# Kernel optimization log

Measured on AMD Instinct MI355X. Metric: run time of the kernel, lower is better.

The kernel has to match this reference:

```python
import jax, jax.numpy as jnp
import numpy as np
import math

N_HEADS, INPUT_DIM, EMBED_DIM = 8, 128, 128
KEY_DIM = EMBED_DIM // N_HEADS  # val_dim = key_dim = 16
B, N = 4, 512


def setup_inputs() -> dict:
    key = jax.random.key(0)
    ks = jax.random.split(key, 8)
    stdv_k = 1.0 / math.sqrt(KEY_DIM)
    stdv_e = 1.0 / math.sqrt(EMBED_DIM)
    stdv_1 = 1.0
    q = jax.random.normal(ks[0], (B, N, INPUT_DIM), dtype=jnp.float32)
    e = jax.random.normal(ks[1], (B, N, N, INPUT_DIM), dtype=jnp.float32)
    W_query = jax.random.uniform(ks[2], (N_HEADS, INPUT_DIM, KEY_DIM), jnp.float32, -stdv_k, stdv_k)
    W_key = jax.random.uniform(ks[3], (N_HEADS, INPUT_DIM, KEY_DIM), jnp.float32, -stdv_k, stdv_k)
    W_val = jax.random.uniform(ks[4], (N_HEADS, INPUT_DIM, KEY_DIM), jnp.float32, -stdv_k, stdv_k)
    E_val1 = jax.random.uniform(ks[5], (N_HEADS, INPUT_DIM, 1), jnp.float32, -stdv_1, stdv_1)
    W_out = jax.random.uniform(ks[6], (N_HEADS, KEY_DIM, EMBED_DIM), jnp.float32, -stdv_e, stdv_e)
    return {"q": q, "e": e, "W_query": W_query, "W_key": W_key,
            "W_val": W_val, "E_val1": E_val1, "W_out": W_out}


def reference(q, e, W_query, W_key, W_val, E_val1, W_out):
    # h = q (self-attention); shapes: q [B,N,D], e [B,N,N,D]
    norm = 1.0 / math.sqrt(W_query.shape[-1])
    Q = jnp.einsum('bnd,hdk->hbnk', q, W_query)  # [H,B,N,k]
    K = jnp.einsum('bnd,hdk->hbnk', q, W_key)
    V = jnp.einsum('bnd,hdv->hbnv', q, W_val)
    # edge bias: per-head scalar projection of edge features -> [H,B,N,N]
    E = jnp.einsum('bnmd,hd->hbnm', e, E_val1[..., 0])
    compat = norm * jnp.einsum('hbnk,hbmk->hbnm', Q, K) + E
    attn = jax.nn.softmax(compat, axis=-1)
    heads = jnp.einsum('hbnm,hbmv->hbnv', attn, V)
    out = jnp.einsum('hbnv,hve->bne', heads, W_out)  # [B,N,embed]
    return out
```

## Files before the change

kernel.cpp:

```cpp
#include <hip/hip_runtime.h>
#include <math.h>

#define BB 4
#define NN 512
#define DD 128
#define HH 8
#define KK 16

__global__ __launch_bounds__(128) void proj_kernel(
    const float* __restrict__ q,
    const float* __restrict__ Wq,
    const float* __restrict__ Wk,
    const float* __restrict__ Wv,
    float* __restrict__ Qs,
    float* __restrict__ Kp,
    float* __restrict__ Vp)
{
    __shared__ float qrow[DD];
    const int bn = blockIdx.x;
    const int t = threadIdx.x;
    qrow[t] = q[(size_t)bn * DD + t];
    __syncthreads();
    const int h = t >> 4;
    const int k = t & 15;
    const float* wq = Wq + (size_t)h * DD * KK + k;
    const float* wk = Wk + (size_t)h * DD * KK + k;
    const float* wv = Wv + (size_t)h * DD * KK + k;
    float aq = 0.f, ak = 0.f, av = 0.f;
#pragma unroll 16
    for (int d = 0; d < DD; ++d) {
        const float x = qrow[d];
        aq = fmaf(x, wq[(size_t)d * KK], aq);
        ak = fmaf(x, wk[(size_t)d * KK], ak);
        av = fmaf(x, wv[(size_t)d * KK], av);
    }
    Qs[(size_t)bn * DD + t] = aq * 0.25f;
    Kp[(size_t)bn * DD + t] = ak;
    Vp[(size_t)bn * DD + t] = av;
}

__global__ __launch_bounds__(256) void attn_kernel(
    const float* __restrict__ e,
    const float* __restrict__ Ev,
    const float* __restrict__ Qs,
    const float* __restrict__ Kp,
    const float* __restrict__ Vp,
    const float* __restrict__ Wout,
    float* __restrict__ out)
{
    __shared__ float comp[HH][NN + 4];
    __shared__ float headsv[HH * KK];

    const int bn   = blockIdx.x;
    const int b    = bn >> 9;
    const int tid  = threadIdx.x;
    const int wave = tid >> 6;
    const int lane = tid & 63;
    const int sub  = lane >> 4;
    const int dc   = lane & 15;
    const int d0   = dc * 8;
    const int myh  = dc >> 1;

    float ev[HH][8];
#pragma unroll
    for (int h = 0; h < HH; ++h) {
        const float4 a = *(const float4*)(Ev + h * DD + d0);
        const float4 c = *(const float4*)(Ev + h * DD + d0 + 4);
        ev[h][0] = a.x; ev[h][1] = a.y; ev[h][2] = a.z; ev[h][3] = a.w;
        ev[h][4] = c.x; ev[h][5] = c.y; ev[h][6] = c.z; ev[h][7] = c.w;
    }
    float qf[8];
    {
        const float4 a = *(const float4*)(Qs + (size_t)bn * DD + d0);
        const float4 c = *(const float4*)(Qs + (size_t)bn * DD + d0 + 4);
        qf[0] = a.x; qf[1] = a.y; qf[2] = a.z; qf[3] = a.w;
        qf[4] = c.x; qf[5] = c.y; qf[6] = c.z; qf[7] = c.w;
    }

    const float* ebase = e  + (size_t)bn * NN * DD;
    const float* kbase = Kp + (size_t)b  * NN * DD;

    for (int i = 0; i < 32; ++i) {
        const int m = wave * 128 + i * 4 + sub;
        const float* ep  = ebase + (size_t)m * DD + d0;
        const float* kpp = kbase + (size_t)m * DD + d0;
        const float4 e0 = *(const float4*)(ep);
        const float4 e1 = *(const float4*)(ep + 4);
        const float4 k0 = *(const float4*)(kpp);
        const float4 k1 = *(const float4*)(kpp + 4);
        float er[8], kr[8];
        er[0] = e0.x; er[1] = e0.y; er[2] = e0.z; er[3] = e0.w;
        er[4] = e1.x; er[5] = e1.y; er[6] = e1.z; er[7] = e1.w;
        kr[0] = k0.x; kr[1] = k0.y; kr[2] = k0.z; kr[3] = k0.w;
        kr[4] = k1.x; kr[5] = k1.y; kr[6] = k1.z; kr[7] = k1.w;

        float kq = 0.f;
#pragma unroll
        for (int j = 0; j < 8; ++j) kq = fmaf(kr[j], qf[j], kq);

        float acc[HH];
#pragma unroll
        for (int h = 0; h < HH; ++h) {
            float s = (myh == h) ? kq : 0.f;
#pragma unroll
            for (int j = 0; j < 8; ++j) s = fmaf(er[j], ev[h][j], s);
            acc[h] = s;
        }

        const bool hi8 = (dc & 8) != 0;
        float t4[4];
#pragma unroll
        for (int j = 0; j < 4; ++j) {
            const float keep = hi8 ? acc[j + 4] : acc[j];
            const float send = hi8 ? acc[j]     : acc[j + 4];
            t4[j] = keep + __shfl_xor(send, 8);
        }
        const bool hi4 = (dc & 4) != 0;
        float t2[2];
#pragma unroll
        for (int j = 0; j < 2; ++j) {
            const float keep = hi4 ? t2[0]*0.f + t4[j + 2] : t4[j];
            const float send = hi4 ? t4[j]     : t4[j + 2];
            t2[j] = keep + __shfl_xor(send, 4);
        }
        const bool hi2 = (dc & 2) != 0;
        float w;
        {
            const float keep = hi2 ? t2[1] : t2[0];
            const float send = hi2 ? t2[0] : t2[1];
            w = keep + __shfl_xor(send, 2);
        }
        w += __shfl_xor(w, 1);
        if ((dc & 1) == 0) comp[dc >> 1][m] = w;
    }
    __syncthreads();

    const float* vbase = Vp + (size_t)b * NN * DD;
#pragma unroll
    for (int hh = 0; hh < 2; ++hh) {
        const int h = wave * 2 + hh;
        float mx = -3.0e38f;
#pragma unroll
        for (int i = 0; i < 8; ++i) mx = fmaxf(mx, comp[h][lane + i * 64]);
#pragma unroll
        for (int mask = 1; mask <= 32; mask <<= 1)
            mx = fmaxf(mx, __shfl_xor(mx, mask));

        float psum = 0.f;
        float av[KK];
#pragma unroll
        for (int v = 0; v < KK; ++v) av[v] = 0.f;
#pragma unroll
        for (int i = 0; i < 8; ++i) {
            const int m = lane + i * 64;
            const float p = __expf(comp[h][m] - mx);
            psum += p;
            const float* vp = vbase + (size_t)m * DD + h * KK;
            const float4 v0 = *(const float4*)(vp);
            const float4 v1 = *(const float4*)(vp + 4);
            const float4 v2 = *(const float4*)(vp + 8);
            const float4 v3 = *(const float4*)(vp + 12);
            av[0]  = fmaf(p, v0.x, av[0]);  av[1]  = fmaf(p, v0.y, av[1]);
            av[2]  = fmaf(p, v0.z, av[2]);  av[3]  = fmaf(p, v0.w, av[3]);
            av[4]  = fmaf(p, v1.x, av[4]);  av[5]  = fmaf(p, v1.y, av[5]);
            av[6]  = fmaf(p, v1.z, av[6]);  av[7]  = fmaf(p, v1.w, av[7]);
            av[8]  = fmaf(p, v2.x, av[8]);  av[9]  = fmaf(p, v2.y, av[9]);
            av[10] = fmaf(p, v2.z, av[10]); av[11] = fmaf(p, v2.w, av[11]);
            av[12] = fmaf(p, v3.x, av[12]); av[13] = fmaf(p, v3.y, av[13]);
            av[14] = fmaf(p, v3.z, av[14]); av[15] = fmaf(p, v3.w, av[15]);
        }
#pragma unroll
        for (int mask = 1; mask <= 32; mask <<= 1)
            psum += __shfl_xor(psum, mask);

        const bool s5 = (lane & 32) != 0;
        float a8[8];
#pragma unroll
        for (int j = 0; j < 8; ++j) {
            const float keep = s5 ? av[j + 8] : av[j];
            const float send = s5 ? av[j]     : av[j + 8];
            a8[j] = keep + __shfl_xor(send, 32);
        }
        const bool s4 = (lane & 16) != 0;
        float a4[4];
#pragma unroll
        for (int j = 0; j < 4; ++j) {
            const float keep = s4 ? a8[j + 4] : a8[j];
            const float send = s4 ? a8[j]     : a8[j + 4];
            a4[j] = keep + __shfl_xor(send, 16);
        }
        const bool s3 = (lane & 8) != 0;
        float a2[2];
#pragma unroll
        for (int j = 0; j < 2; ++j) {
            const float keep = s3 ? a4[j + 2] : a4[j];
            const float send = s3 ? a4[j]     : a4[j + 2];
            a2[j] = keep + __shfl_xor(send, 8);
        }
        const bool s2 = (lane & 4) != 0;
        float a1;
        {
            const float keep = s2 ? a2[1] : a2[0];
            const float send = s2 ? a2[0] : a2[1];
            a1 = keep + __shfl_xor(send, 4);
        }
        a1 += __shfl_xor(a1, 2);
        a1 += __shfl_xor(a1, 1);
        if ((lane & 3) == 0)
            headsv[h * KK + (lane >> 2)] = a1 / psum;
    }
    __syncthreads();

    if (tid < DD) {
        float o = 0.f;
#pragma unroll 8
        for (int p = 0; p < HH * KK; ++p)
            o = fmaf(headsv[p], Wout[(size_t)p * DD + tid], o);
        out[(size_t)bn * DD + tid] = o;
    }
}

extern "C" void kernel_launch(void* const* d_in, const int* in_sizes, int n_in,
                              void* d_out, int out_size, void* d_ws, size_t ws_size,
                              hipStream_t stream) {
    const float* q    = (const float*)d_in[0];
    const float* e    = (const float*)d_in[1];
    const float* Wq   = (const float*)d_in[2];
    const float* Wk   = (const float*)d_in[3];
    const float* Wv   = (const float*)d_in[4];
    const float* Ev   = (const float*)d_in[5];
    const float* Wout = (const float*)d_in[6];
    float* out = (float*)d_out;

    float* Qs = (float*)d_ws;
    float* Kp = Qs + (size_t)BB * NN * DD;
    float* Vp = Kp + (size_t)BB * NN * DD;

    proj_kernel<<<BB * NN, 128, 0, stream>>>(q, Wq, Wk, Wv, Qs, Kp, Vp);
    attn_kernel<<<BB * NN, 256, 0, stream>>>(e, Ev, Qs, Kp, Vp, Wout, out);
}
```

Baseline: 222.5 us.

## Remap edge-score lanes to float4 per row and software-pipeline loads

The edge/key scoring loop now has each lane handle 4 features (32 lanes per row, 2 rows per wave pass) instead of 8. Loads are double-buffered in registers so the next pair of rows is fetched while the current pair is reduced. The launch bounds also ask for 4 blocks per SM to cap register use. This is meant to hide global-memory latency on the large edge tensor, in exchange for more shuffle steps per row and tighter register pressure.

```diff
diff --git a/kernel.cpp b/kernel.cpp
--- a/kernel.cpp
+++ b/kernel.cpp
@@ -39,7 +39,7 @@
     Vp[(size_t)bn * DD + t] = av;
 }
 
-__global__ __launch_bounds__(256) void attn_kernel(
+__global__ __launch_bounds__(256, 4) void attn_kernel(
     const float* __restrict__ e,
     const float* __restrict__ Ev,
     const float* __restrict__ Qs,
@@ -56,83 +56,92 @@
     const int tid  = threadIdx.x;
     const int wave = tid >> 6;
     const int lane = tid & 63;
-    const int sub  = lane >> 4;
-    const int dc   = lane & 15;
-    const int d0   = dc * 8;
-    const int myh  = dc >> 1;
-
-    float ev[HH][8];
+    const int r    = lane >> 5;
+    const int c    = lane & 31;
+    const int d0   = c * 4;
+    const int myh  = c >> 2;
+    const int hidx = (c >> 2) & 7;
+
+    float ev[HH][4];
 #pragma unroll
     for (int h = 0; h < HH; ++h) {
         const float4 a = *(const float4*)(Ev + h * DD + d0);
-        const float4 c = *(const float4*)(Ev + h * DD + d0 + 4);
         ev[h][0] = a.x; ev[h][1] = a.y; ev[h][2] = a.z; ev[h][3] = a.w;
-        ev[h][4] = c.x; ev[h][5] = c.y; ev[h][6] = c.z; ev[h][7] = c.w;
-    }
-    float qf[8];
-    {
-        const float4 a = *(const float4*)(Qs + (size_t)bn * DD + d0);
-        const float4 c = *(const float4*)(Qs + (size_t)bn * DD + d0 + 4);
-        qf[0] = a.x; qf[1] = a.y; qf[2] = a.z; qf[3] = a.w;
-        qf[4] = c.x; qf[5] = c.y; qf[6] = c.z; qf[7] = c.w;
-    }
-
-    const float* ebase = e  + (size_t)bn * NN * DD;
-    const float* kbase = Kp + (size_t)b  * NN * DD;
-
-    for (int i = 0; i < 32; ++i) {
-        const int m = wave * 128 + i * 4 + sub;
-        const float* ep  = ebase + (size_t)m * DD + d0;
-        const float* kpp = kbase + (size_t)m * DD + d0;
-        const float4 e0 = *(const float4*)(ep);
-        const float4 e1 = *(const float4*)(ep + 4);
-        const float4 k0 = *(const float4*)(kpp);
-        const float4 k1 = *(const float4*)(kpp + 4);
-        float er[8], kr[8];
-        er[0] = e0.x; er[1] = e0.y; er[2] = e0.z; er[3] = e0.w;
-        er[4] = e1.x; er[5] = e1.y; er[6] = e1.z; er[7] = e1.w;
-        kr[0] = k0.x; kr[1] = k0.y; kr[2] = k0.z; kr[3] = k0.w;
-        kr[4] = k1.x; kr[5] = k1.y; kr[6] = k1.z; kr[7] = k1.w;
-
-        float kq = 0.f;
-#pragma unroll
-        for (int j = 0; j < 8; ++j) kq = fmaf(kr[j], qf[j], kq);
-
+    }
+    const float4 qf = *(const float4*)(Qs + (size_t)bn * DD + d0);
+
+    const int mb = wave * 128 + r;
+    const float* epl = e  + (size_t)bn * NN * DD + (size_t)mb * DD + d0;
+    const float* kpl = Kp + (size_t)b  * NN * DD + (size_t)mb * DD + d0;
+
+    const bool f16 = (c & 16) != 0;
+    const bool f8  = (c & 8)  != 0;
+    const bool f4  = (c & 4)  != 0;
+
+    auto do_pass = [&](const float4 ee, const float4 kk, const int m) {
+        float kq;
+        kq = kk.x * qf.x;
+        kq = fmaf(kk.y, qf.y, kq);
+        kq = fmaf(kk.z, qf.z, kq);
+        kq = fmaf(kk.w, qf.w, kq);
         float acc[HH];
 #pragma unroll
         for (int h = 0; h < HH; ++h) {
             float s = (myh == h) ? kq : 0.f;
-#pragma unroll
-            for (int j = 0; j < 8; ++j) s = fmaf(er[j], ev[h][j], s);
+            s = fmaf(ee.x, ev[h][0], s);
+            s = fmaf(ee.y, ev[h][1], s);
+            s = fmaf(ee.z, ev[h][2], s);
+            s = fmaf(ee.w, ev[h][3], s);
             acc[h] = s;
         }
-
-        const bool hi8 = (dc & 8) != 0;
         float t4[4];
 #pragma unroll
         for (int j = 0; j < 4; ++j) {
-            const float keep = hi8 ? acc[j + 4] : acc[j];
-            const float send = hi8 ? acc[j]     : acc[j + 4];
-            t4[j] = keep + __shfl_xor(send, 8);
-        }
-        const bool hi4 = (dc & 4) != 0;
+            const float keep = f16 ? acc[j + 4] : acc[j];
+            const float send = f16 ? acc[j]     : acc[j + 4];
+            t4[j] = keep + __shfl_xor(send, 16);
+        }
         float t2[2];
 #pragma unroll
         for (int j = 0; j < 2; ++j) {
-            const float keep = hi4 ? t2[0]*0.f + t4[j + 2] : t4[j];
-            const float send = hi4 ? t4[j]     : t4[j + 2];
-            t2[j] = keep + __shfl_xor(send, 4);
-        }
-        const bool hi2 = (dc & 2) != 0;
+            const float keep = f8 ? t4[j + 2] : t4[j];
+            const float send = f8 ? t4[j]     : t4[j + 2];
+            t2[j] = keep + __shfl_xor(send, 8);
+        }
         float w;
         {
-            const float keep = hi2 ? t2[1] : t2[0];
-            const float send = hi2 ? t2[0] : t2[1];
-            w = keep + __shfl_xor(send, 2);
-        }
+            const float keep = f4 ? t2[1] : t2[0];
+            const float send = f4 ? t2[0] : t2[1];
+            w = keep + __shfl_xor(send, 4);
+        }
+        w += __shfl_xor(w, 2);
         w += __shfl_xor(w, 1);
-        if ((dc & 1) == 0) comp[dc >> 1][m] = w;
-    }
+        if ((c & 3) == 0) comp[hidx][m] = w;
+    };
+
+#define LDF4(p, base) (*(const float4*)((base) + (size_t)(p) * 256))
+
+    float4 ea0 = LDF4(0, epl), ea1 = LDF4(1, epl);
+    float4 ka0 = LDF4(0, kpl), ka1 = LDF4(1, kpl);
+    float4 eb0, eb1, kb0, kb1;
+
+    for (int g = 0; g < 32; g += 2) {
+        {
+            const int p0 = 2 * g + 2, p1 = 2 * g + 3;
+            eb0 = LDF4(p0, epl); eb1 = LDF4(p1, epl);
+            kb0 = LDF4(p0, kpl); kb1 = LDF4(p1, kpl);
+        }
+        do_pass(ea0, ka0, mb + 4 * g);
+        do_pass(ea1, ka1, mb + 4 * g + 2);
+        if (g + 2 < 32) {
+            const int p0 = 2 * g + 4, p1 = 2 * g + 5;
+            ea0 = LDF4(p0, epl); ea1 = LDF4(p1, epl);
+            ka0 = LDF4(p0, kpl); ka1 = LDF4(p1, kpl);
+        }
+        do_pass(eb0, kb0, mb + 4 * g + 4);
+        do_pass(eb1, kb1, mb + 4 * g + 6);
+    }
+#undef LDF4
     __syncthreads();
 
     const float* vbase = Vp + (size_t)b * NN * DD;
```

After: 229.8 us. 1.03x slower.

## Precompute QK^T and transposed V; software-pipeline edge-feature loads in attention

Applied to the files above, without the earlier changes.

Moves the per-head Q·K dot products into a separate kernel that reuses four query rows per block, so the attention kernel streams only the edge tensor in its main loop. V is transposed so the softmax-weighted sum reads coalesced rows. The edge loads are triple-buffered in registers to overlap memory latency with the per-head reductions. In exchange it adds two kernel launches and writes and reads a QK^T buffer of B*N*H*N floats (about 32 MB) to workspace.

```diff
diff --git a/kernel.cpp b/kernel.cpp
--- a/kernel.cpp
+++ b/kernel.cpp
@@ -39,12 +39,78 @@
     Vp[(size_t)bn * DD + t] = av;
 }
 
+__global__ __launch_bounds__(256) void vt_kernel(
+    const float* __restrict__ Vp, float* __restrict__ Vt)
+{
+    __shared__ float tile[64][129];
+    const int b  = blockIdx.x >> 3;
+    const int m0 = (blockIdx.x & 7) * 64;
+    const int t  = threadIdx.x;
+    const float* src = Vp + ((size_t)b * NN + m0) * DD;
+#pragma unroll
+    for (int j = 0; j < 8; ++j) {
+        const int idx4 = t + j * 256;
+        const float4 v = *(const float4*)(src + (size_t)idx4 * 4);
+        const int r = idx4 >> 5, c = (idx4 & 31) * 4;
+        tile[r][c] = v.x; tile[r][c+1] = v.y; tile[r][c+2] = v.z; tile[r][c+3] = v.w;
+    }
+    __syncthreads();
+    const int m = t & 63;
+#pragma unroll
+    for (int p0 = 0; p0 < 128; p0 += 4) {
+        const int p = p0 + (t >> 6);
+        Vt[((size_t)b * DD + p) * NN + m0 + m] = tile[m][p];
+    }
+}
+
+__global__ __launch_bounds__(256) void qkt_kernel(
+    const float* __restrict__ Qs, const float* __restrict__ Kp,
+    float* __restrict__ QKT)
+{
+    const int b    = blockIdx.x >> 7;
+    const int n4   = blockIdx.x & 127;
+    const int tid  = threadIdx.x;
+    const int wave = tid >> 6;
+    const int lane = tid & 63;
+    const int sub  = lane >> 4;
+    const int dc   = lane & 15;
+    const int d0   = dc * 8;
+
+    float qf[4][8];
+#pragma unroll
+    for (int j = 0; j < 4; ++j) {
+        const float* qp = Qs + ((size_t)b * NN + n4 * 4 + j) * DD + d0;
+        const float4 a = *(const float4*)qp;
+        const float4 c = *(const float4*)(qp + 4);
+        qf[j][0]=a.x; qf[j][1]=a.y; qf[j][2]=a.z; qf[j][3]=a.w;
+        qf[j][4]=c.x; qf[j][5]=c.y; qf[j][6]=c.z; qf[j][7]=c.w;
+    }
+    const float* kbase = Kp + (size_t)b * NN * DD;
+    for (int i = 0; i < 32; ++i) {
+        const int m = wave * 128 + i * 4 + sub;
+        const float* kp = kbase + (size_t)m * DD + d0;
+        const float4 k0 = *(const float4*)kp;
+        const float4 k1 = *(const float4*)(kp + 4);
+        float kr[8];
+        kr[0]=k0.x; kr[1]=k0.y; kr[2]=k0.z; kr[3]=k0.w;
+        kr[4]=k1.x; kr[5]=k1.y; kr[6]=k1.z; kr[7]=k1.w;
+#pragma unroll
+        for (int j = 0; j < 4; ++j) {
+            float s = kr[0] * qf[j][0];
+#pragma unroll
+            for (int u = 1; u < 8; ++u) s = fmaf(kr[u], qf[j][u], s);
+            s += __shfl_xor(s, 1);
+            if ((dc & 1) == 0)
+                QKT[(((size_t)b * NN + n4 * 4 + j) * HH + (dc >> 1)) * NN + m] = s;
+        }
+    }
+}
+
 __global__ __launch_bounds__(256) void attn_kernel(
     const float* __restrict__ e,
     const float* __restrict__ Ev,
-    const float* __restrict__ Qs,
-    const float* __restrict__ Kp,
-    const float* __restrict__ Vp,
+    const float* __restrict__ QKT,
+    const float* __restrict__ Vt,
     const float* __restrict__ Wout,
     float* __restrict__ out)
 {
@@ -59,55 +125,34 @@
     const int sub  = lane >> 4;
     const int dc   = lane & 15;
     const int d0   = dc * 8;
-    const int myh  = dc >> 1;
 
     float ev[HH][8];
 #pragma unroll
     for (int h = 0; h < HH; ++h) {
         const float4 a = *(const float4*)(Ev + h * DD + d0);
         const float4 c = *(const float4*)(Ev + h * DD + d0 + 4);
-        ev[h][0] = a.x; ev[h][1] = a.y; ev[h][2] = a.z; ev[h][3] = a.w;
-        ev[h][4] = c.x; ev[h][5] = c.y; ev[h][6] = c.z; ev[h][7] = c.w;
-    }
-    float qf[8];
-    {
-        const float4 a = *(const float4*)(Qs + (size_t)bn * DD + d0);
-        const float4 c = *(const float4*)(Qs + (size_t)bn * DD + d0 + 4);
-        qf[0] = a.x; qf[1] = a.y; qf[2] = a.z; qf[3] = a.w;
-        qf[4] = c.x; qf[5] = c.y; qf[6] = c.z; qf[7] = c.w;
-    }
-
-    const float* ebase = e  + (size_t)bn * NN * DD;
-    const float* kbase = Kp + (size_t)b  * NN * DD;
-
-    for (int i = 0; i < 32; ++i) {
-        const int m = wave * 128 + i * 4 + sub;
-        const float* ep  = ebase + (size_t)m * DD + d0;
-        const float* kpp = kbase + (size_t)m * DD + d0;
-        const float4 e0 = *(const float4*)(ep);
-        const float4 e1 = *(const float4*)(ep + 4);
-        const float4 k0 = *(const float4*)(kpp);
-        const float4 k1 = *(const float4*)(kpp + 4);
-        float er[8], kr[8];
-        er[0] = e0.x; er[1] = e0.y; er[2] = e0.z; er[3] = e0.w;
-        er[4] = e1.x; er[5] = e1.y; er[6] = e1.z; er[7] = e1.w;
-        kr[0] = k0.x; kr[1] = k0.y; kr[2] = k0.z; kr[3] = k0.w;
-        kr[4] = k1.x; kr[5] = k1.y; kr[6] = k1.z; kr[7] = k1.w;
-
-        float kq = 0.f;
-#pragma unroll
-        for (int j = 0; j < 8; ++j) kq = fmaf(kr[j], qf[j], kq);
-
+        ev[h][0]=a.x; ev[h][1]=a.y; ev[h][2]=a.z; ev[h][3]=a.w;
+        ev[h][4]=c.x; ev[h][5]=c.y; ev[h][6]=c.z; ev[h][7]=c.w;
+    }
+
+    const bool hi8 = (dc & 8) != 0;
+    const bool hi4 = (dc & 4) != 0;
+    const bool hi2 = (dc & 2) != 0;
+    const float* epl = e + (size_t)bn * NN * DD
+                         + (size_t)(wave * 128 + sub) * DD + d0;
+
+    auto do_pass = [&](const float4 e0, const float4 e1, const int p) {
+        float er[8];
+        er[0]=e0.x; er[1]=e0.y; er[2]=e0.z; er[3]=e0.w;
+        er[4]=e1.x; er[5]=e1.y; er[6]=e1.z; er[7]=e1.w;
         float acc[HH];
 #pragma unroll
         for (int h = 0; h < HH; ++h) {
-            float s = (myh == h) ? kq : 0.f;
-#pragma unroll
-            for (int j = 0; j < 8; ++j) s = fmaf(er[j], ev[h][j], s);
+            float s = er[0] * ev[h][0];
+#pragma unroll
+            for (int u = 1; u < 8; ++u) s = fmaf(er[u], ev[h][u], s);
             acc[h] = s;
         }
-
-        const bool hi8 = (dc & 8) != 0;
         float t4[4];
 #pragma unroll
         for (int j = 0; j < 4; ++j) {
@@ -115,15 +160,13 @@
             const float send = hi8 ? acc[j]     : acc[j + 4];
             t4[j] = keep + __shfl_xor(send, 8);
         }
-        const bool hi4 = (dc & 4) != 0;
         float t2[2];
 #pragma unroll
         for (int j = 0; j < 2; ++j) {
-            const float keep = hi4 ? t2[0]*0.f + t4[j + 2] : t4[j];
+            const float keep = hi4 ? t4[j + 2] : t4[j];
             const float send = hi4 ? t4[j]     : t4[j + 2];
             t2[j] = keep + __shfl_xor(send, 4);
         }
-        const bool hi2 = (dc & 2) != 0;
         float w;
         {
             const float keep = hi2 ? t2[1] : t2[0];
@@ -131,43 +174,54 @@
             w = keep + __shfl_xor(send, 2);
         }
         w += __shfl_xor(w, 1);
-        if ((dc & 1) == 0) comp[dc >> 1][m] = w;
-    }
-    __syncthreads();
-
-    const float* vbase = Vp + (size_t)b * NN * DD;
+        if ((dc & 1) == 0) comp[dc >> 1][wave * 128 + p * 4 + sub] = w;
+    };
+
+#define LDE(B0, B1, p) { const float* _p = epl + (size_t)(p) * 512; \
+                         B0 = *(const float4*)_p; B1 = *(const float4*)(_p + 4); }
+
+    float4 A0, A1, B0, B1, C0, C1;
+    LDE(A0, A1, 0); LDE(B0, B1, 1);
+    for (int p = 0; p < 30; p += 3) {
+        LDE(C0, C1, p + 2); do_pass(A0, A1, p);
+        LDE(A0, A1, p + 3); do_pass(B0, B1, p + 1);
+        LDE(B0, B1, p + 4); do_pass(C0, C1, p + 2);
+    }
+    do_pass(A0, A1, 30); do_pass(B0, B1, 31);
+#undef LDE
+    __syncthreads();
+
 #pragma unroll
     for (int hh = 0; hh < 2; ++hh) {
         const int h = wave * 2 + hh;
-        float mx = -3.0e38f;
-#pragma unroll
-        for (int i = 0; i < 8; ++i) mx = fmaxf(mx, comp[h][lane + i * 64]);
+        const float* qk   = QKT + ((size_t)bn * HH + h) * NN;
+        const float* vrow = Vt + ((size_t)b * DD + h * KK) * NN;
+
+        float s[8];
+#pragma unroll
+        for (int i = 0; i < 8; ++i)
+            s[i] = comp[h][lane + i * 64] + qk[lane + i * 64];
+
+        float mx = s[0];
+#pragma unroll
+        for (int i = 1; i < 8; ++i) mx = fmaxf(mx, s[i]);
 #pragma unroll
         for (int mask = 1; mask <= 32; mask <<= 1)
             mx = fmaxf(mx, __shfl_xor(mx, mask));
 
-        float psum = 0.f;
+        float pr[8], psum = 0.f;
+#pragma unroll
+        for (int i = 0; i < 8; ++i) { pr[i] = __expf(s[i] - mx); psum += pr[i]; }
+
         float av[KK];
 #pragma unroll
         for (int v = 0; v < KK; ++v) av[v] = 0.f;
 #pragma unroll
-        for (int i = 0; i < 8; ++i) {
-            const int m = lane + i * 64;
-            const float p = __expf(comp[h][m] - mx);
-            psum += p;
-            const float* vp = vbase + (size_t)m * DD + h * KK;
-            const float4 v0 = *(const float4*)(vp);
-            const float4 v1 = *(const float4*)(vp + 4);
-            const float4 v2 = *(const float4*)(vp + 8);
-            const float4 v3 = *(const float4*)(vp + 12);
-            av[0]  = fmaf(p, v0.x, av[0]);  av[1]  = fmaf(p, v0.y, av[1]);
-            av[2]  = fmaf(p, v0.z, av[2]);  av[3]  = fmaf(p, v0.w, av[3]);
-            av[4]  = fmaf(p, v1.x, av[4]);  av[5]  = fmaf(p, v1.y, av[5]);
-            av[6]  = fmaf(p, v1.z, av[6]);  av[7]  = fmaf(p, v1.w, av[7]);
-            av[8]  = fmaf(p, v2.x, av[8]);  av[9]  = fmaf(p, v2.y, av[9]);
-            av[10] = fmaf(p, v2.z, av[10]); av[11] = fmaf(p, v2.w, av[11]);
-            av[12] = fmaf(p, v3.x, av[12]); av[13] = fmaf(p, v3.y, av[13]);
-            av[14] = fmaf(p, v3.z, av[14]); av[15] = fmaf(p, v3.w, av[15]);
+        for (int v = 0; v < KK; ++v) {
+            const float* vp = vrow + (size_t)v * NN + lane;
+#pragma unroll
+            for (int i = 0; i < 8; ++i)
+                av[v] = fmaf(pr[i], vp[i * 64], av[v]);
         }
 #pragma unroll
         for (int mask = 1; mask <= 32; mask <<= 1)
@@ -232,10 +286,14 @@
     const float* Wout = (const float*)d_in[6];
     float* out = (float*)d_out;
 
-    float* Qs = (float*)d_ws;
-    float* Kp = Qs + (size_t)BB * NN * DD;
-    float* Vp = Kp + (size_t)BB * NN * DD;
+    float* Qs  = (float*)d_ws;
+    float* Kp  = Qs  + (size_t)BB * NN * DD;
+    float* Vp  = Kp  + (size_t)BB * NN * DD;
+    float* Vt  = Vp  + (size_t)BB * NN * DD;
+    float* QKT = Vt  + (size_t)BB * DD * NN;
 
     proj_kernel<<<BB * NN, 128, 0, stream>>>(q, Wq, Wk, Wv, Qs, Kp, Vp);
-    attn_kernel<<<BB * NN, 256, 0, stream>>>(e, Ev, Qs, Kp, Vp, Wout, out);
-}
+    vt_kernel<<<BB * 8, 256, 0, stream>>>(Vp, Vt);
+    qkt_kernel<<<BB * 128, 256, 0, stream>>>(Qs, Kp, QKT);
+    attn_kernel<<<BB * NN, 256, 0, stream>>>(e, Ev, QKT, Vt, Wout, out);
+}
```

Result: faster. 200.7 us (-9.8%).
